# Performance work log

Hardware: AMD Instinct MI355X
Metric: run time of the kernel (lower is better)

## Reference

```python
import jax, jax.numpy as jnp
import numpy as np

S, B, H = 2048, 32, 1024

def setup_inputs() -> dict:
    key = jax.random.key(0)
    k1, k2, k3 = jax.random.split(key, 3)
    hidden = jax.random.normal(k1, (1, B, H), dtype=jnp.float32)
    encoder_outputs = jax.random.normal(k2, (S, B, H), dtype=jnp.float32)
    W = jax.random.normal(k3, (H, H), dtype=jnp.float32) * (1.0 / np.sqrt(H))
    b = jnp.zeros((H,), dtype=jnp.float32)
    return {"hidden": hidden, "encoder_outputs": encoder_outputs, "W": W, "b": b}

def reference(hidden, encoder_outputs, W, b):
    # method == 'general': energy[b,i] = hidden[0,b] . (W @ enc[i,b] + bias)
    # proj: [S, B, H] = enc @ W^T + b  (nn.Linear convention: y = x W^T + b)
    proj = jnp.einsum('sbh,kh->sbk', encoder_outputs, W) + b
    # scores: [B, S]
    scores = jnp.einsum('bh,sbh->bs', hidden[0], proj)
    attn = jax.nn.softmax(scores, axis=1)
    return attn[:, None, :]  # [B, 1, S]
```

## Files before the change

kernel.cpp:

```cpp
#include <hip/hip_runtime.h>
#include <math.h>

#define H 1024
#define S 2048
#define B 32

__global__ void __launch_bounds__(512)
proj_hidden_kernel(const float* __restrict__ hidden,
                   const float* __restrict__ W,
                   float* __restrict__ v) {
    __shared__ float hs[2][H];
    __shared__ float part[32][2][64];
    const int hc = blockIdx.x & 15;
    const int bg = blockIdx.x >> 4;
    const int hq = threadIdx.x & 15;
    const int kg = threadIdx.x >> 4;

    for (int i = threadIdx.x; i < 2 * H; i += 512)
        hs[i >> 10][i & 1023] = hidden[(bg * 2 + (i >> 10)) * H + (i & 1023)];
    __syncthreads();

    const int h = hc * 64 + hq * 4;
    float4 a0 = {0.f, 0.f, 0.f, 0.f};
    float4 a1 = {0.f, 0.f, 0.f, 0.f};
#pragma unroll 4
    for (int kk = 0; kk < 32; ++kk) {
        const int k = kg + 32 * kk;
        const float h0 = hs[0][k];
        const float h1 = hs[1][k];
        const float4 w = *reinterpret_cast<const float4*>(W + (size_t)k * H + h);
        a0.x = fmaf(h0, w.x, a0.x); a0.y = fmaf(h0, w.y, a0.y);
        a0.z = fmaf(h0, w.z, a0.z); a0.w = fmaf(h0, w.w, a0.w);
        a1.x = fmaf(h1, w.x, a1.x); a1.y = fmaf(h1, w.y, a1.y);
        a1.z = fmaf(h1, w.z, a1.z); a1.w = fmaf(h1, w.w, a1.w);
    }
    *reinterpret_cast<float4*>(&part[kg][0][hq * 4]) = a0;
    *reinterpret_cast<float4*>(&part[kg][1][hq * 4]) = a1;
    __syncthreads();

    if (threadIdx.x < 128) {
        const int bb = threadIdx.x >> 6;
        const int c  = threadIdx.x & 63;
        float sum = 0.f;
#pragma unroll 8
        for (int g = 0; g < 32; ++g) sum += part[g][bb][c];
        v[(bg * 2 + bb) * H + hc * 64 + c] = sum;
    }
}

__global__ void __launch_bounds__(256)
scores_kernel(const float* __restrict__ enc,
              const float* __restrict__ v,
              float* __restrict__ scores) {
    const int b     = blockIdx.x & 31;
    const int strip = blockIdx.x >> 5;
    const int wave  = threadIdx.x >> 6;
    const int lane  = threadIdx.x & 63;

    const float4* vb = reinterpret_cast<const float4*>(v + (size_t)b * H);
    float4 vf0 = vb[lane];
    float4 vf1 = vb[lane + 64];
    float4 vf2 = vb[lane + 128];
    float4 vf3 = vb[lane + 192];

    const int s_base = strip * 64 + wave * 16;
    const float4* enc4 = reinterpret_cast<const float4*>(enc);

    for (int i = 0; i < 16; i += 4) {
        const int s = s_base + i;
        const float4* r0 = enc4 + ((size_t)(s + 0) * B + b) * 256;
        const float4* r1 = enc4 + ((size_t)(s + 1) * B + b) * 256;
        const float4* r2 = enc4 + ((size_t)(s + 2) * B + b) * 256;
        const float4* r3 = enc4 + ((size_t)(s + 3) * B + b) * 256;

        float a0 = 0.f, a1 = 0.f, a2 = 0.f, a3 = 0.f;
#define ROWQ(acc, rp, q, vf)                                            \
        {                                                               \
            const float4 e = rp[lane + 64 * q];                         \
            acc = fmaf(e.x, vf.x, fmaf(e.y, vf.y,                       \
                  fmaf(e.z, vf.z, fmaf(e.w, vf.w, acc))));              \
        }
        ROWQ(a0, r0, 0, vf0) ROWQ(a0, r0, 1, vf1) ROWQ(a0, r0, 2, vf2) ROWQ(a0, r0, 3, vf3)
        ROWQ(a1, r1, 0, vf0) ROWQ(a1, r1, 1, vf1) ROWQ(a1, r1, 2, vf2) ROWQ(a1, r1, 3, vf3)
        ROWQ(a2, r2, 0, vf0) ROWQ(a2, r2, 1, vf1) ROWQ(a2, r2, 2, vf2) ROWQ(a2, r2, 3, vf3)
        ROWQ(a3, r3, 0, vf0) ROWQ(a3, r3, 1, vf1) ROWQ(a3, r3, 2, vf2) ROWQ(a3, r3, 3, vf3)
#undef ROWQ

#pragma unroll
        for (int off = 32; off > 0; off >>= 1) {
            a0 += __shfl_down(a0, off, 64);
            a1 += __shfl_down(a1, off, 64);
            a2 += __shfl_down(a2, off, 64);
            a3 += __shfl_down(a3, off, 64);
        }
        if (lane == 0) {
            float4 r = {a0, a1, a2, a3};
            *reinterpret_cast<float4*>(scores + (size_t)b * S + s) = r;
        }
    }
}

__global__ void __launch_bounds__(256)
softmax_kernel(const float* __restrict__ scores,
               float* __restrict__ out) {
    const int b    = blockIdx.x;
    const int tid  = threadIdx.x;
    const int wave = tid >> 6;
    const int lane = tid & 63;

    __shared__ float wmax[4];
    __shared__ float wsum[4];

    float x[8];
    float m = -INFINITY;
#pragma unroll
    for (int i = 0; i < 8; ++i) {
        x[i] = scores[(size_t)b * S + tid + i * 256];
        m = fmaxf(m, x[i]);
    }
#pragma unroll
    for (int off = 32; off > 0; off >>= 1)
        m = fmaxf(m, __shfl_down(m, off, 64));
    if (lane == 0) wmax[wave] = m;
    __syncthreads();
    m = fmaxf(fmaxf(wmax[0], wmax[1]), fmaxf(wmax[2], wmax[3]));

    float sum = 0.f;
#pragma unroll
    for (int i = 0; i < 8; ++i) {
        x[i] = __expf(x[i] - m);
        sum += x[i];
    }
#pragma unroll
    for (int off = 32; off > 0; off >>= 1)
        sum += __shfl_down(sum, off, 64);
    if (lane == 0) wsum[wave] = sum;
    __syncthreads();
    sum = (wsum[0] + wsum[1]) + (wsum[2] + wsum[3]);

    const float inv = 1.0f / sum;
#pragma unroll
    for (int i = 0; i < 8; ++i) {
        out[(size_t)b * S + tid + i * 256] = x[i] * inv;
    }
}

extern "C" void kernel_launch(void* const* d_in, const int* in_sizes, int n_in,
                              void* d_out, int out_size, void* d_ws, size_t ws_size,
                              hipStream_t stream) {
    const float* hidden = (const float*)d_in[0];
    const float* enc    = (const float*)d_in[1];
    const float* W      = (const float*)d_in[2];

    float* v      = (float*)d_ws;
    float* scores = v + (size_t)B * H;
    float* out    = (float*)d_out;

    proj_hidden_kernel<<<256, 512, 0, stream>>>(hidden, W, v);
    scores_kernel<<<1024, 256, 0, stream>>>(enc, v, scores);
    softmax_kernel<<<B, 256, 0, stream>>>(scores, out);
}
```

Before: 59.70 us.

## Stream contiguous encoder rows per block and stage all hidden projections in LDS

The scores kernel now gives each 512-thread block 128 consecutive (s,b) rows of the encoder tensor, so its reads are one contiguous stream instead of rows strided by B*H. To make that work, each block first copies the whole projected hidden matrix v (32x1024 floats, 128 KB) into dynamic shared memory. Each row then looks up its batch vector there, and scores are written as scattered scalars. The cost is a 128 KB LDS fill per block, which adds L2 traffic and limits each CU to one block. The kernel also depends on a dynamic shared allocation that large being accepted at launch.

Measured after the change: 61.99 us. 1.04x slower.

```diff
diff --git a/kernel.cpp b/kernel.cpp
--- a/kernel.cpp
+++ b/kernel.cpp
@@ -48,44 +48,42 @@
     }
 }
 
-__global__ void __launch_bounds__(256)
+__global__ void __launch_bounds__(512)
 scores_kernel(const float* __restrict__ enc,
               const float* __restrict__ v,
               float* __restrict__ scores) {
-    const int b     = blockIdx.x & 31;
-    const int strip = blockIdx.x >> 5;
-    const int wave  = threadIdx.x >> 6;
-    const int lane  = threadIdx.x & 63;
+    extern __shared__ float vlds[];
+    const int wave = threadIdx.x >> 6;
+    const int lane = threadIdx.x & 63;
 
-    const float4* vb = reinterpret_cast<const float4*>(v + (size_t)b * H);
-    float4 vf0 = vb[lane];
-    float4 vf1 = vb[lane + 64];
-    float4 vf2 = vb[lane + 128];
-    float4 vf3 = vb[lane + 192];
+    {
+        const float4* v4 = reinterpret_cast<const float4*>(v);
+        float4* s4 = reinterpret_cast<float4*>(vlds);
+        for (int i = threadIdx.x; i < (32 * H) / 4; i += 512)
+            s4[i] = v4[i];
+    }
+    __syncthreads();
 
-    const int s_base = strip * 64 + wave * 16;
-    const float4* enc4 = reinterpret_cast<const float4*>(enc);
+    const size_t g0 = (size_t)blockIdx.x * 128 + (size_t)wave * 16;
+    const float4* enc4 = reinterpret_cast<const float4*>(enc) + g0 * (H / 4);
 
     for (int i = 0; i < 16; i += 4) {
-        const int s = s_base + i;
-        const float4* r0 = enc4 + ((size_t)(s + 0) * B + b) * 256;
-        const float4* r1 = enc4 + ((size_t)(s + 1) * B + b) * 256;
-        const float4* r2 = enc4 + ((size_t)(s + 2) * B + b) * 256;
-        const float4* r3 = enc4 + ((size_t)(s + 3) * B + b) * 256;
-
         float a0 = 0.f, a1 = 0.f, a2 = 0.f, a3 = 0.f;
-#define ROWQ(acc, rp, q, vf)                                            \
-        {                                                               \
-            const float4 e = rp[lane + 64 * q];                         \
-            acc = fmaf(e.x, vf.x, fmaf(e.y, vf.y,                       \
-                  fmaf(e.z, vf.z, fmaf(e.w, vf.w, acc))));              \
+#define ROW(acc, r)                                                          \
+        {                                                                    \
+            const float4* ep = enc4 + (size_t)(i + (r)) * (H / 4);           \
+            const int b = (int)((g0 + i + (r)) & 31);                        \
+            const float4* vp = reinterpret_cast<const float4*>(vlds + b * H);\
+            _Pragma("unroll")                                                \
+            for (int q = 0; q < 4; ++q) {                                    \
+                const float4 e = ep[lane + 64 * q];                          \
+                const float4 w = vp[lane + 64 * q];                          \
+                acc = fmaf(e.x, w.x, fmaf(e.y, w.y,                          \
+                      fmaf(e.z, w.z, fmaf(e.w, w.w, acc))));                 \
+            }                                                                \
         }
-        ROWQ(a0, r0, 0, vf0) ROWQ(a0, r0, 1, vf1) ROWQ(a0, r0, 2, vf2) ROWQ(a0, r0, 3, vf3)
-        ROWQ(a1, r1, 0, vf0) ROWQ(a1, r1, 1, vf1) ROWQ(a1, r1, 2, vf2) ROWQ(a1, r1, 3, vf3)
-        ROWQ(a2, r2, 0, vf0) ROWQ(a2, r2, 1, vf1) ROWQ(a2, r2, 2, vf2) ROWQ(a2, r2, 3, vf3)
-        ROWQ(a3, r3, 0, vf0) ROWQ(a3, r3, 1, vf1) ROWQ(a3, r3, 2, vf2) ROWQ(a3, r3, 3, vf3)
-#undef ROWQ
-
+        ROW(a0, 0) ROW(a1, 1) ROW(a2, 2) ROW(a3, 3)
+#undef ROW
 #pragma unroll
         for (int off = 32; off > 0; off >>= 1) {
             a0 += __shfl_down(a0, off, 64);
@@ -94,8 +92,11 @@
             a3 += __shfl_down(a3, off, 64);
         }
         if (lane == 0) {
-            float4 r = {a0, a1, a2, a3};
-            *reinterpret_cast<float4*>(scores + (size_t)b * S + s) = r;
+            const size_t g = g0 + i;
+            scores[((g + 0) & 31) * S + ((g + 0) >> 5)] = a0;
+            scores[((g + 1) & 31) * S + ((g + 1) >> 5)] = a1;
+            scores[((g + 2) & 31) * S + ((g + 2) >> 5)] = a2;
+            scores[((g + 3) & 31) * S + ((g + 3) >> 5)] = a3;
         }
     }
 }
@@ -157,6 +158,6 @@
     float* out    = (float*)d_out;
 
     proj_hidden_kernel<<<256, 512, 0, stream>>>(hidden, W, v);
-    scores_kernel<<<1024, 256, 0, stream>>>(enc, v, scores);
+    scores_kernel<<<512, 512, 32 * H * sizeof(float), stream>>>(enc, v, scores);
     softmax_kernel<<<B, 256, 0, stream>>>(scores, out);
 }
```
